# Performance work log

Measured on AMD Instinct MI355X. Metric: run time of the kernel, lower is better.

## Reference

```python
import jax, jax.numpy as jnp
import numpy as np

OUT_H, OUT_W = 7, 7
SPATIAL_SCALE = 0.125
SAMPLING_RATIO = 2


def setup_inputs() -> dict:
    key = jax.random.key(0)
    k1, k2, k3, k4 = jax.random.split(key, 4)
    inputs = jax.random.normal(k1, (2, 100, 100, 256), dtype=jnp.float32)
    # boxes in image coords (stride-8 feature over ~800px image): x0,y0,x1,y1
    xy0 = jax.random.uniform(k2, (1024, 2), minval=0.0, maxval=600.0)
    wh = jax.random.uniform(k3, (1024, 2), minval=8.0, maxval=200.0)
    boxes = jnp.concatenate([xy0, xy0 + wh], axis=1).astype(jnp.float32)
    box_inds = jax.random.randint(k4, (1024,), 0, 2, dtype=jnp.int32)
    return {"inputs": inputs, "boxes": boxes, "box_inds": box_inds}


def _roi_align(inputs, boxes, box_inds):
    """aligned=True ROIAlign: crop_and_resize at oversampled grid + avg pool.

    Sample coordinate (per aligned=True transform + tf.crop_and_resize):
      x_j = x0*scale + spacing_w*(j+0.5) - 0.5, spacing_w = w_box*scale/crop_w
    Out-of-range samples get extrapolation_value=0 (TF semantics).
    """
    N, H, W, C = inputs.shape
    B = boxes.shape[0]
    ch, cw = OUT_H * SAMPLING_RATIO, OUT_W * SAMPLING_RATIO

    sb = boxes * SPATIAL_SCALE
    x0, y0, x1, y1 = sb[:, 0], sb[:, 1], sb[:, 2], sb[:, 3]
    sw = (x1 - x0) / cw  # [B]
    sh = (y1 - y0) / ch
    xs = x0[:, None] + sw[:, None] * (jnp.arange(cw, dtype=sb.dtype) + 0.5) - 0.5  # [B,cw]
    ys = y0[:, None] + sh[:, None] * (jnp.arange(ch, dtype=sb.dtype) + 0.5) - 0.5  # [B,ch]

    yl = jnp.floor(ys)
    xl = jnp.floor(xs)
    ty = ys - yl  # [B,ch]
    tx = xs - xl  # [B,cw]
    yli = jnp.clip(yl, 0, H - 1).astype(jnp.int32)
    yhi = jnp.clip(yl + 1, 0, H - 1).astype(jnp.int32)
    xli = jnp.clip(xl, 0, W - 1).astype(jnp.int32)
    xhi = jnp.clip(xl + 1, 0, W - 1).astype(jnp.int32)

    b = box_inds[:, None, None]

    def g(yy, xx):  # gather -> [B,ch,cw,C]
        return inputs[b, yy[:, :, None], xx[:, None, :], :]

    txe = tx[:, None, :, None]
    top = g(yli, xli) * (1.0 - txe) + g(yli, xhi) * txe
    bot = g(yhi, xli) * (1.0 - txe) + g(yhi, xhi) * txe
    tye = ty[:, :, None, None]
    out = top * (1.0 - tye) + bot * tye  # [B,ch,cw,C]

    valid = ((ys >= 0) & (ys <= H - 1))[:, :, None] & ((xs >= 0) & (xs <= W - 1))[:, None, :]
    out = jnp.where(valid[..., None], out, 0.0)

    # avg_pool2d kernel=stride=SAMPLING_RATIO (SAME==VALID since exact multiple)
    out = out.reshape(B, OUT_H, SAMPLING_RATIO, OUT_W, SAMPLING_RATIO, C).mean(axis=(2, 4))
    return out  # [B, OUT_H, OUT_W, C]


def reference(inputs, boxes, box_inds):
    return _roi_align(inputs, boxes, box_inds)
```

## Files before the change

### kernel.cpp

```cpp
#include <hip/hip_runtime.h>


constexpr int   H_IN  = 100;
constexpr int   W_IN  = 100;
constexpr int   C_IN  = 256;
constexpr int   OUT_H = 7;
constexpr int   OUT_W = 7;
constexpr int   NPIX  = OUT_H * OUT_W;
constexpr int   NBOX  = 1024;
constexpr float SCALE = 0.125f;

typedef float f32x4 __attribute__((ext_vector_type(4)));

struct Meta { int4 off; float4 w; };

constexpr int RMETA_OFF = 4096;
constexpr int CMETA_OFF = 4096 + 7168 * 32;

__global__ __launch_bounds__(1024) void sort_boxes_kernel(
    const float* __restrict__ boxes,
    const int*   __restrict__ box_inds,
    int*         __restrict__ perm)
{
    const int tid  = threadIdx.x;
    const int wave = tid >> 6;
    const int lane = tid & 63;

    const float y0 = boxes[tid * 4 + 1] * SCALE;
    const float y1 = boxes[tid * 4 + 3] * SCALE;
    const float cy = 0.5f * (y0 + y1);
    int band = (int)(cy * (1.0f / 25.0f));
    band = min(max(band, 0), 3);
    const int bin = box_inds[tid] * 4 + band;

    __shared__ int whist[16][8];
    __shared__ int wbase[16][8];

    int wrank = 0;
    const unsigned long long ltmask = (lane == 63) ? ~0ull >> 1
                                                   : (1ull << lane) - 1;
#pragma unroll
    for (int k = 0; k < 8; ++k) {
        const unsigned long long bal = __ballot(bin == k);
        if (bin == k) wrank = __popcll(bal & ltmask);
        if (lane == 0) whist[wave][k] = __popcll(bal);
    }
    __syncthreads();

    if (tid == 0) {
        int acc = 0;
        for (int k = 0; k < 8; ++k)
            for (int w = 0; w < 16; ++w) {
                wbase[w][k] = acc;
                acc += whist[w][k];
            }
    }
    __syncthreads();

    perm[wbase[wave][bin] + wrank] = tid;
}

__device__ __forceinline__ int merge_dim(float s0, float s1, int LIM,
                                         int* idx, float* w)
{
    const float f0 = floorf(s0);
    const float f1 = floorf(s1);
    const float t0 = s0 - f0;
    const float t1 = s1 - f1;
    const float va = (s0 >= 0.0f && s0 <= (float)(LIM - 1)) ? 1.0f : 0.0f;
    const float vb = (s1 >= 0.0f && s1 <= (float)(LIM - 1)) ? 1.0f : 0.0f;
    const int i0 = (int)f0;
    const int i1 = (int)f1;

    int n;
    if (i1 == i0) {
        n = 2;
        idx[0] = i0;     w[0] = va * (1.0f - t0) + vb * (1.0f - t1);
        idx[1] = i0 + 1; w[1] = va * t0 + vb * t1;
        idx[2] = i0;     w[2] = 0.0f;
        idx[3] = i0;     w[3] = 0.0f;
    } else if (i1 == i0 + 1) {
        n = 3;
        idx[0] = i0;     w[0] = va * (1.0f - t0);
        idx[1] = i0 + 1; w[1] = va * t0 + vb * (1.0f - t1);
        idx[2] = i0 + 2; w[2] = vb * t1;
        idx[3] = i0;     w[3] = 0.0f;
    } else {
        n = 4;
        idx[0] = i0;     w[0] = va * (1.0f - t0);
        idx[1] = i0 + 1; w[1] = va * t0;
        idx[2] = i1;     w[2] = vb * (1.0f - t1);
        idx[3] = i1 + 1; w[3] = vb * t1;
    }
#pragma unroll
    for (int k = 0; k < 4; ++k)
        idx[k] = min(max(idx[k], 0), LIM - 1);
    return n;
}

__global__ __launch_bounds__(256) void meta_kernel(
    const float* __restrict__ boxes,
    const int*   __restrict__ box_inds,
    const int*   __restrict__ perm,
    Meta*        __restrict__ rmeta,
    Meta*        __restrict__ cmeta)
{
    const int t = blockIdx.x * 256 + threadIdx.x;
    if (t >= NBOX * 14) return;
    const int slot = t / 14;
    const int d    = t - slot * 14;

    const int b = perm[slot];
    const int n = box_inds[b];

    const float bx0 = boxes[b * 4 + 0] * SCALE;
    const float by0 = boxes[b * 4 + 1] * SCALE;
    const float bx1 = boxes[b * 4 + 2] * SCALE;
    const float by1 = boxes[b * 4 + 3] * SCALE;
    const float sw  = (bx1 - bx0) * (1.0f / 14.0f);
    const float sh  = (by1 - by0) * (1.0f / 14.0f);

    int idx[4]; float wgt[4];
    Meta m;
    if (d < 7) {
        const float s0 = by0 + sh * ((float)(d * 2) + 0.5f) - 0.5f;
        const int   nr = merge_dim(s0, s0 + sh, H_IN, idx, wgt);
#pragma unroll
        for (int k = 0; k < 4; ++k) {
            ((int*)&m.off)[k]  = n * (H_IN * W_IN * C_IN) + idx[k] * (W_IN * C_IN);
            ((float*)&m.w)[k]  = wgt[k] * 0.25f;
        }
        m.off.x |= (nr - 2);
        rmeta[slot * 7 + d] = m;
    } else {
        const int   ox = d - 7;
        const float s0 = bx0 + sw * ((float)(ox * 2) + 0.5f) - 0.5f;
        const int   nc = merge_dim(s0, s0 + sw, W_IN, idx, wgt);
#pragma unroll
        for (int k = 0; k < 4; ++k) {
            ((int*)&m.off)[k]  = idx[k] * C_IN;
            ((float*)&m.w)[k]  = wgt[k];
        }
        m.off.x |= (nc - 2);
        cmeta[slot * 7 + ox] = m;
    }
}

template<int NR, int NC>
__device__ __forceinline__ f32x4 gather(const float* __restrict__ base,
                                        const int* ro, const int* co,
                                        const float* wr, const float* wc,
                                        int c4)
{
    f32x4 v[NR * NC];
#pragma unroll
    for (int i = 0; i < NR; ++i)
#pragma unroll
        for (int j = 0; j < NC; ++j)
            v[i * NC + j] = *(const f32x4*)(base + (size_t)(ro[i] + co[j] + c4));

    f32x4 acc = {0.f, 0.f, 0.f, 0.f};
#pragma unroll
    for (int i = 0; i < NR; ++i)
#pragma unroll
        for (int j = 0; j < NC; ++j)
            acc += v[i * NC + j] * (wr[i] * wc[j]);
    return acc;
}

__global__ __launch_bounds__(256) void roi_align_kernel(
    const float* __restrict__ inputs,
    const int*   __restrict__ perm,
    const Meta*  __restrict__ rmeta,
    const Meta*  __restrict__ cmeta,
    float*       __restrict__ out)
{
    const int lane = threadIdx.x & 63;
    const int sub  = __builtin_amdgcn_readfirstlane(threadIdx.x >> 6);

    const int nchunk = gridDim.x >> 3;
    const int lbid   = (blockIdx.x & 7) * nchunk + (blockIdx.x >> 3);
    const int p      = lbid * 4 + sub;

    const int bs  = p / NPIX;
    const int rem = p - bs * NPIX;
    const int oy  = (rem * 37) >> 8;
    const int ox  = rem - oy * 7;

    const int b = __builtin_amdgcn_readfirstlane(perm[bs]);

    Meta rm = rmeta[bs * 7 + oy];
    Meta cm = cmeta[bs * 7 + ox];

    const int sel = __builtin_amdgcn_readfirstlane(
        (rm.off.x & 3) * 3 + (cm.off.x & 3));
    rm.off.x &= ~3;
    cm.off.x &= ~3;

    const int* ro   = (const int*)&rm.off;
    const float* wr = (const float*)&rm.w;
    const int* co   = (const int*)&cm.off;
    const float* wc = (const float*)&cm.w;
    const int c4 = lane * 4;

    f32x4 acc;
    switch (sel) {
        case 0: acc = gather<2, 2>(inputs, ro, co, wr, wc, c4); break;
        case 1: acc = gather<2, 3>(inputs, ro, co, wr, wc, c4); break;
        case 2: acc = gather<2, 4>(inputs, ro, co, wr, wc, c4); break;
        case 3: acc = gather<3, 2>(inputs, ro, co, wr, wc, c4); break;
        case 4: acc = gather<3, 3>(inputs, ro, co, wr, wc, c4); break;
        case 5: acc = gather<3, 4>(inputs, ro, co, wr, wc, c4); break;
        case 6: acc = gather<4, 2>(inputs, ro, co, wr, wc, c4); break;
        case 7: acc = gather<4, 3>(inputs, ro, co, wr, wc, c4); break;
        default: acc = gather<4, 4>(inputs, ro, co, wr, wc, c4); break;
    }

    float* op = out + ((size_t)b * NPIX + rem) * C_IN + c4;
    __builtin_nontemporal_store(acc, (f32x4*)op);
}

extern "C" void kernel_launch(void* const* d_in, const int* in_sizes, int n_in,
                              void* d_out, int out_size, void* d_ws, size_t ws_size,
                              hipStream_t stream) {
    const float* inputs   = (const float*)d_in[0];
    const float* boxes    = (const float*)d_in[1];
    const int*   box_inds = (const int*)d_in[2];
    float*       out      = (float*)d_out;

    int*  perm  = (int*)d_ws;
    Meta* rmeta = (Meta*)((char*)d_ws + RMETA_OFF);
    Meta* cmeta = (Meta*)((char*)d_ws + CMETA_OFF);

    sort_boxes_kernel<<<1, NBOX, 0, stream>>>(boxes, box_inds, perm);
    meta_kernel<<<56, 256, 0, stream>>>(boxes, box_inds, perm, rmeta, cmeta);

    const int blocks = NBOX * NPIX / 4;
    roi_align_kernel<<<blocks, 256, 0, stream>>>(inputs, perm, rmeta, cmeta, out);
}
```

Before: 31.16 us.

## Process half output rows per wave with column register ring reuse

Each wave now computes 3-4 adjacent output pixels along a row instead of one. Loaded input columns go into a 4-slot register ring, so columns shared by neighbouring pixels are fetched only once. The row and column weights are folded into a contiguous span with only valid samples kept, and the block prefix in the sort kernel becomes a parallel scan. This cuts redundant global loads but gives the grid fewer waves, adds a serial loop per wave, and uses more registers.

```diff
diff --git a/kernel.cpp b/kernel.cpp
--- a/kernel.cpp
+++ b/kernel.cpp
@@ -34,7 +34,7 @@
     const int bin = box_inds[tid] * 4 + band;
 
     __shared__ int whist[16][8];
-    __shared__ int wbase[16][8];
+    __shared__ int sc[129];
 
     int wrank = 0;
     const unsigned long long ltmask = (lane == 63) ? ~0ull >> 1
@@ -47,55 +47,52 @@
     }
     __syncthreads();
 
-    if (tid == 0) {
-        int acc = 0;
-        for (int k = 0; k < 8; ++k)
-            for (int w = 0; w < 16; ++w) {
-                wbase[w][k] = acc;
-                acc += whist[w][k];
-            }
-    }
+    if (tid < 128) sc[tid + 1] = whist[tid & 15][tid >> 4];
+    if (tid == 0)  sc[0] = 0;
     __syncthreads();
-
-    perm[wbase[wave][bin] + wrank] = tid;
-}
-
-__device__ __forceinline__ int merge_dim(float s0, float s1, int LIM,
-                                         int* idx, float* w)
-{
-    const float f0 = floorf(s0);
-    const float f1 = floorf(s1);
-    const float t0 = s0 - f0;
-    const float t1 = s1 - f1;
-    const float va = (s0 >= 0.0f && s0 <= (float)(LIM - 1)) ? 1.0f : 0.0f;
-    const float vb = (s1 >= 0.0f && s1 <= (float)(LIM - 1)) ? 1.0f : 0.0f;
-    const int i0 = (int)f0;
-    const int i1 = (int)f1;
-
-    int n;
-    if (i1 == i0) {
-        n = 2;
-        idx[0] = i0;     w[0] = va * (1.0f - t0) + vb * (1.0f - t1);
-        idx[1] = i0 + 1; w[1] = va * t0 + vb * t1;
-        idx[2] = i0;     w[2] = 0.0f;
-        idx[3] = i0;     w[3] = 0.0f;
-    } else if (i1 == i0 + 1) {
-        n = 3;
-        idx[0] = i0;     w[0] = va * (1.0f - t0);
-        idx[1] = i0 + 1; w[1] = va * t0 + vb * (1.0f - t1);
-        idx[2] = i0 + 2; w[2] = vb * t1;
-        idx[3] = i0;     w[3] = 0.0f;
-    } else {
-        n = 4;
-        idx[0] = i0;     w[0] = va * (1.0f - t0);
-        idx[1] = i0 + 1; w[1] = va * t0;
-        idx[2] = i1;     w[2] = vb * (1.0f - t1);
-        idx[3] = i1 + 1; w[3] = vb * t1;
-    }
-#pragma unroll
-    for (int k = 0; k < 4; ++k)
-        idx[k] = min(max(idx[k], 0), LIM - 1);
-    return n;
+    for (int off = 1; off < 128; off <<= 1) {
+        int v = 0;
+        if (tid < 128 && tid >= off) v = sc[tid - off + 1];
+        __syncthreads();
+        if (tid < 128 && tid >= off) sc[tid + 1] += v;
+        __syncthreads();
+    }
+
+    perm[sc[bin * 16 + wave] + wrank] = tid;
+}
+
+__device__ __forceinline__ void fold_dim(float s0, float step, int LIM,
+                                         int& c0, int& n, float* w)
+{
+    float s[2] = { s0, s0 + step };
+    int   fl[2]; float t[2]; bool val[2];
+    int lo = 0x7fffffff, hi = -0x7fffffff;
+#pragma unroll
+    for (int k = 0; k < 2; ++k) {
+        const float f = floorf(s[k]);
+        fl[k]  = (int)f;
+        t[k]   = s[k] - f;
+        val[k] = (s[k] >= 0.0f && s[k] <= (float)(LIM - 1));
+        if (val[k]) {
+            lo = min(lo, fl[k]);
+            hi = max(hi, min(fl[k] + 1, LIM - 1));
+        }
+    }
+    w[0] = w[1] = w[2] = w[3] = 0.0f;
+    if (lo > hi) {
+        c0 = min(max(fl[0], 0), LIM - 1);
+        n  = 1;
+        return;
+    }
+    c0 = lo;
+    n  = hi - lo + 1;
+#pragma unroll
+    for (int k = 0; k < 2; ++k) {
+        if (val[k]) {
+            w[fl[k] - lo]                    += 1.0f - t[k];
+            w[min(fl[k] + 1, LIM - 1) - lo]  += t[k];
+        }
+    }
 }
 
 __global__ __launch_bounds__(256) void meta_kernel(
@@ -120,52 +117,85 @@
     const float sw  = (bx1 - bx0) * (1.0f / 14.0f);
     const float sh  = (by1 - by0) * (1.0f / 14.0f);
 
-    int idx[4]; float wgt[4];
+    int c0, cnt; float wgt[4];
     Meta m;
+    m.off.y = m.off.z = m.off.w = 0;
     if (d < 7) {
         const float s0 = by0 + sh * ((float)(d * 2) + 0.5f) - 0.5f;
-        const int   nr = merge_dim(s0, s0 + sh, H_IN, idx, wgt);
-#pragma unroll
-        for (int k = 0; k < 4; ++k) {
-            ((int*)&m.off)[k]  = n * (H_IN * W_IN * C_IN) + idx[k] * (W_IN * C_IN);
-            ((float*)&m.w)[k]  = wgt[k] * 0.25f;
-        }
-        m.off.x |= (nr - 2);
+        fold_dim(s0, sh, H_IN, c0, cnt, wgt);
+        m.off.x = (n * (H_IN * W_IN * C_IN) + c0 * (W_IN * C_IN)) | (cnt - 1);
+        m.w.x = wgt[0] * 0.25f; m.w.y = wgt[1] * 0.25f;
+        m.w.z = wgt[2] * 0.25f; m.w.w = wgt[3] * 0.25f;
         rmeta[slot * 7 + d] = m;
     } else {
-        const int   ox = d - 7;
+        const int ox = d - 7;
         const float s0 = bx0 + sw * ((float)(ox * 2) + 0.5f) - 0.5f;
-        const int   nc = merge_dim(s0, s0 + sw, W_IN, idx, wgt);
-#pragma unroll
-        for (int k = 0; k < 4; ++k) {
-            ((int*)&m.off)[k]  = idx[k] * C_IN;
-            ((float*)&m.w)[k]  = wgt[k];
-        }
-        m.off.x |= (nc - 2);
+        fold_dim(s0, sw, W_IN, c0, cnt, wgt);
+        m.off.x = (c0 << 3) | cnt;
+        m.w.x = wgt[0]; m.w.y = wgt[1]; m.w.z = wgt[2]; m.w.w = wgt[3];
         cmeta[slot * 7 + ox] = m;
     }
 }
 
-template<int NR, int NC>
-__device__ __forceinline__ f32x4 gather(const float* __restrict__ base,
-                                        const int* ro, const int* co,
-                                        const float* wr, const float* wc,
-                                        int c4)
-{
-    f32x4 v[NR * NC];
-#pragma unroll
-    for (int i = 0; i < NR; ++i)
-#pragma unroll
-        for (int j = 0; j < NC; ++j)
-            v[i * NC + j] = *(const f32x4*)(base + (size_t)(ro[i] + co[j] + c4));
-
-    f32x4 acc = {0.f, 0.f, 0.f, 0.f};
-#pragma unroll
-    for (int i = 0; i < NR; ++i)
-#pragma unroll
-        for (int j = 0; j < NC; ++j)
-            acc += v[i * NC + j] * (wr[i] * wc[j]);
-    return acc;
+template<int NR>
+__device__ __forceinline__ void process_half(
+    const float* __restrict__ inputs,
+    const Meta*  __restrict__ cmeta,
+    float*       __restrict__ out,
+    int slotbase, int r0off, const float* wr,
+    int b, int oy, int ox0, int npx, int c4)
+{
+    f32x4 ring[4][NR];
+#pragma unroll
+    for (int s = 0; s < 4; ++s)
+#pragma unroll
+        for (int r = 0; r < NR; ++r)
+            ring[s][r] = f32x4{0.f, 0.f, 0.f, 0.f};
+
+    int L = -1000000;
+
+    for (int j = 0; j < npx; ++j) {
+        const int ox = ox0 + j;
+        const Meta cm = cmeta[slotbase + ox];
+        const int pk = __builtin_amdgcn_readfirstlane(cm.off.x);
+        const int c0 = pk >> 3;
+        const int nc = pk & 7;
+        const int lo = max(L, c0);
+        const int hi = c0 + nc;
+
+#pragma unroll
+        for (int s = 0; s < 4; ++s) {
+            const int cs = lo + ((s - lo) & 3);
+            if (cs < hi) {
+                const int cb = r0off + cs * C_IN + c4;
+#pragma unroll
+                for (int r = 0; r < NR; ++r)
+                    ring[s][r] = *(const f32x4*)(inputs + cb + r * (W_IN * C_IN));
+            }
+        }
+        L = hi > L ? hi : L;
+
+        const float w0 = cm.w.x, w1 = cm.w.y, w2 = cm.w.z, w3 = cm.w.w;
+        float ws0, ws1, ws2, ws3;
+        switch (c0 & 3) {
+            case 0:  ws0 = w0; ws1 = w1; ws2 = w2; ws3 = w3; break;
+            case 1:  ws0 = w3; ws1 = w0; ws2 = w1; ws3 = w2; break;
+            case 2:  ws0 = w2; ws1 = w3; ws2 = w0; ws3 = w1; break;
+            default: ws0 = w1; ws1 = w2; ws2 = w3; ws3 = w0; break;
+        }
+
+        f32x4 acc = {0.f, 0.f, 0.f, 0.f};
+#pragma unroll
+        for (int r = 0; r < NR; ++r) {
+            acc += ring[0][r] * (wr[r] * ws0);
+            acc += ring[1][r] * (wr[r] * ws1);
+            acc += ring[2][r] * (wr[r] * ws2);
+            acc += ring[3][r] * (wr[r] * ws3);
+        }
+
+        float* op = out + ((size_t)b * NPIX + oy * OUT_W + ox) * C_IN + c4;
+        __builtin_nontemporal_store(acc, (f32x4*)op);
+    }
 }
 
 __global__ __launch_bounds__(256) void roi_align_kernel(
@@ -176,48 +206,36 @@
     float*       __restrict__ out)
 {
     const int lane = threadIdx.x & 63;
-    const int sub  = __builtin_amdgcn_readfirstlane(threadIdx.x >> 6);
+    const int wv   = threadIdx.x >> 6;
 
     const int nchunk = gridDim.x >> 3;
     const int lbid   = (blockIdx.x & 7) * nchunk + (blockIdx.x >> 3);
-    const int p      = lbid * 4 + sub;
-
-    const int bs  = p / NPIX;
-    const int rem = p - bs * NPIX;
-    const int oy  = (rem * 37) >> 8;
-    const int ox  = rem - oy * 7;
-
-    const int b = __builtin_amdgcn_readfirstlane(perm[bs]);
-
-    Meta rm = rmeta[bs * 7 + oy];
-    Meta cm = cmeta[bs * 7 + ox];
-
-    const int sel = __builtin_amdgcn_readfirstlane(
-        (rm.off.x & 3) * 3 + (cm.off.x & 3));
-    rm.off.x &= ~3;
-    cm.off.x &= ~3;
-
-    const int* ro   = (const int*)&rm.off;
-    const float* wr = (const float*)&rm.w;
-    const int* co   = (const int*)&cm.off;
-    const float* wc = (const float*)&cm.w;
+    const int wgid   = lbid * 4 + wv;
+
+    const int slot = wgid / 14;
+    const int d    = wgid - slot * 14;
+    const int oy   = d >> 1;
+    const int half = d & 1;
+    const int ox0  = half ? 4 : 0;
+    const int npx  = half ? 3 : 4;
+
+    const int b = __builtin_amdgcn_readfirstlane(perm[slot]);
+
+    const Meta rm = rmeta[slot * 7 + oy];
+    const int rpk   = __builtin_amdgcn_readfirstlane(rm.off.x);
+    const int nrm1  = rpk & 3;
+    const int r0off = rpk & ~3;
+    const float wr[4] = { rm.w.x, rm.w.y, rm.w.z, rm.w.w };
+
     const int c4 = lane * 4;
-
-    f32x4 acc;
-    switch (sel) {
-        case 0: acc = gather<2, 2>(inputs, ro, co, wr, wc, c4); break;
-        case 1: acc = gather<2, 3>(inputs, ro, co, wr, wc, c4); break;
-        case 2: acc = gather<2, 4>(inputs, ro, co, wr, wc, c4); break;
-        case 3: acc = gather<3, 2>(inputs, ro, co, wr, wc, c4); break;
-        case 4: acc = gather<3, 3>(inputs, ro, co, wr, wc, c4); break;
-        case 5: acc = gather<3, 4>(inputs, ro, co, wr, wc, c4); break;
-        case 6: acc = gather<4, 2>(inputs, ro, co, wr, wc, c4); break;
-        case 7: acc = gather<4, 3>(inputs, ro, co, wr, wc, c4); break;
-        default: acc = gather<4, 4>(inputs, ro, co, wr, wc, c4); break;
-    }
-
-    float* op = out + ((size_t)b * NPIX + rem) * C_IN + c4;
-    __builtin_nontemporal_store(acc, (f32x4*)op);
+    const int slotbase = slot * 7;
+
+    switch (nrm1) {
+        case 0:  process_half<1>(inputs, cmeta, out, slotbase, r0off, wr, b, oy, ox0, npx, c4); break;
+        case 1:  process_half<2>(inputs, cmeta, out, slotbase, r0off, wr, b, oy, ox0, npx, c4); break;
+        case 2:  process_half<3>(inputs, cmeta, out, slotbase, r0off, wr, b, oy, ox0, npx, c4); break;
+        default: process_half<4>(inputs, cmeta, out, slotbase, r0off, wr, b, oy, ox0, npx, c4); break;
+    }
 }
 
 extern "C" void kernel_launch(void* const* d_in, const int* in_sizes, int n_in,
@@ -235,6 +253,6 @@
     sort_boxes_kernel<<<1, NBOX, 0, stream>>>(boxes, box_inds, perm);
     meta_kernel<<<56, 256, 0, stream>>>(boxes, box_inds, perm, rmeta, cmeta);
 
-    const int blocks = NBOX * NPIX / 4;
+    const int blocks = NBOX * 14 / 4;
     roi_align_kernel<<<blocks, 256, 0, stream>>>(inputs, perm, rmeta, cmeta, out);
 }
```

After: 34.10 us. 9.4% more time.
